# Kernel tuning notes

Hardware: AMD Instinct MI355X
Metric: run time of the kernel (lower is better)

The kernel has to match this reference:

```python
import jax, jax.numpy as jnp
import numpy as np

N, E = 50000, 800000
IN, H1, H2, HEADS, EMB = 128, 32, 32, 4, 128
NEG_SLOPE = 0.2  # DGL GATConv default leaky_relu slope


def setup_inputs() -> dict:
    key = jax.random.key(0)
    ks = jax.random.split(key, 14)
    s = 0.05
    return {
        "x": jax.random.normal(ks[0], (N, IN), jnp.float32),
        "src": jax.random.randint(ks[1], (E,), 0, N, jnp.int32),
        "dst": jax.random.randint(ks[2], (E,), 0, N, jnp.int32),
        "W1": jax.random.normal(ks[3], (IN, HEADS * H1), jnp.float32) * s,
        "al1": jax.random.normal(ks[4], (HEADS, H1), jnp.float32) * s,
        "ar1": jax.random.normal(ks[5], (HEADS, H1), jnp.float32) * s,
        "b1": jnp.zeros((HEADS * H1,), jnp.float32),
        "W2": jax.random.normal(ks[6], (HEADS * H1, HEADS * H2), jnp.float32) * s,
        "al2": jax.random.normal(ks[7], (HEADS, H2), jnp.float32) * s,
        "ar2": jax.random.normal(ks[8], (HEADS, H2), jnp.float32) * s,
        "b2": jnp.zeros((HEADS * H2,), jnp.float32),
        "Wp": jax.random.normal(ks[9], (HEADS * H2, EMB), jnp.float32) * s,
        "bp": jnp.zeros((EMB,), jnp.float32),
    }


def gat_layer(x, W, al, ar, b, src, dst, heads, d_out):
    n = x.shape[0]
    feat = (x @ W).reshape(n, heads, d_out)            # [N,H,D]
    el = (feat * al).sum(-1)                           # [N,H]
    er = (feat * ar).sum(-1)                           # [N,H]
    e = jax.nn.leaky_relu(el[src] + er[dst], NEG_SLOPE)  # [E,H]
    # edge softmax over destination segments
    m = jax.ops.segment_max(e, dst, num_segments=n)    # [N,H] (-inf for empty)
    ex = jnp.exp(e - m[dst])                           # [E,H]
    z = jax.ops.segment_sum(ex, dst, num_segments=n)   # [N,H]
    alpha = ex / z[dst]                                # [E,H]
    msg = alpha[:, :, None] * feat[src]                # [E,H,D]
    out = jax.ops.segment_sum(msg, dst, num_segments=n)  # [N,H,D]
    return out + b.reshape(1, heads, d_out)


def reference(x, src, dst, W1, al1, ar1, b1, W2, al2, ar2, b2, Wp, bp):
    h = gat_layer(x, W1, al1, ar1, b1, src, dst, HEADS, H1).reshape(N, -1)
    h = gat_layer(h, W2, al2, ar2, b2, src, dst, HEADS, H2).reshape(N, -1)
    out = h @ Wp + bp
    return (h, out)
```

## Files before the change

### kernel.cpp

```cpp
#include <hip/hip_runtime.h>
#include <hip/hip_bf16.h>

#define N_NODES 50000
#define HEADS 4
#define DHEAD 32
#define F 128
#define NEG_SLOPE 0.2f

typedef unsigned int uint;
typedef unsigned short ushort;
typedef __attribute__((ext_vector_type(8))) short bf16x8;
typedef __attribute__((ext_vector_type(4))) float f32x4;

__device__ __forceinline__ float bf2f(ushort u) {
    union { uint i; float f; } c; c.i = ((uint)u) << 16; return c.f;
}
__device__ __forceinline__ ushort f2bf(float f) {
    union { float f; uint i; } c; c.f = f;
    uint u = c.i + 0x7FFF + ((c.i >> 16) & 1);
    return (ushort)(u >> 16);
}

__global__ void rank_hist_kernel(const int* __restrict__ dst, int* __restrict__ counts,
                                 int* __restrict__ rank, int E) {
    int i = blockIdx.x * 256 + threadIdx.x;
    if (i < E) rank[i] = atomicAdd(&counts[dst[i]], 1);
}

__global__ __launch_bounds__(256) void scanA_kernel(const int* __restrict__ counts,
                                                    int* __restrict__ local_sc,
                                                    int* __restrict__ partials, int N) {
    int i = blockIdx.x * 256 + threadIdx.x;
    int v = (i < N) ? counts[i] : 0;
    int lane = threadIdx.x & 63;
    int w = threadIdx.x >> 6;
    int x = v;
#pragma unroll
    for (int off = 1; off < 64; off <<= 1) {
        int t = __shfl_up(x, off);
        if (lane >= off) x += t;
    }
    __shared__ int wsum[4];
    if (lane == 63) wsum[w] = x;
    __syncthreads();
    int wpre = 0;
#pragma unroll
    for (int k = 0; k < 4; k++)
        if (k < w) wpre += wsum[k];
    if (i < N) local_sc[i] = x - v + wpre;
    if (threadIdx.x == 255) partials[blockIdx.x] = wpre + x;
}

__global__ void scanB_kernel(int* __restrict__ partials, int NP) {
    int tid = threadIdx.x;
    int v = (tid < NP) ? partials[tid] : 0;
    int lane = tid & 63;
    int w = tid >> 6;
    int x = v;
#pragma unroll
    for (int off = 1; off < 64; off <<= 1) {
        int t = __shfl_up(x, off);
        if (lane >= off) x += t;
    }
    __shared__ int wsum[4];
    if (lane == 63) wsum[w] = x;
    __syncthreads();
    int wpre = 0;
#pragma unroll
    for (int k = 0; k < 4; k++)
        if (k < w) wpre += wsum[k];
    if (tid < NP) partials[tid] = x - v + wpre;
}

__global__ __launch_bounds__(256) void scanC_kernel(int* __restrict__ offs,
                                                    const int* __restrict__ partials,
                                                    int N, int E) {
    int i = blockIdx.x * 256 + threadIdx.x;
    if (i < N) offs[i] += partials[blockIdx.x];
    if (i == 0) offs[N] = E;
}

__global__ void posfix_kernel(const int* __restrict__ dst, const int* __restrict__ offs,
                              int* __restrict__ rank, int E) {
    int i = blockIdx.x * 256 + threadIdx.x;
    if (i < E) rank[i] += offs[dst[i]];
}

#define SCH 2048
__global__ __launch_bounds__(256) void scatter_ranged_kernel(
    const int* __restrict__ src, const int* __restrict__ pos,
    int* __restrict__ csr_src, int E) {
    int range = blockIdx.x & 7;
    int chunk = blockIdx.x >> 3;
    int base = chunk * SCH + threadIdx.x;
    int lo = (int)(((long long)range * E) >> 3);
    int hi = (int)(((long long)(range + 1) * E) >> 3);
#pragma unroll
    for (int k = 0; k < SCH / 256; k++) {
        int i = base + k * 256;
        if (i < E) {
            int p = pos[i];
            if (p >= lo && p < hi) csr_src[p] = src[i];
        }
    }
}

__global__ __launch_bounds__(256) void wtrans_kernel(const float* __restrict__ W1,
                                                     const float* __restrict__ W2,
                                                     const float* __restrict__ Wp,
                                                     ushort* __restrict__ WT) {
    const float* W = (blockIdx.x == 0) ? W1 : (blockIdx.x == 1) ? W2 : Wp;
    ushort* T = WT + (size_t)blockIdx.x * 128 * 128;
    for (int i = threadIdx.x; i < 128 * 128; i += 256) {
        int r = i >> 7, c = i & 127;
        T[c * 128 + r] = f2bf(W[i]);
    }
}

template <bool A_FP32, bool OUT_BF16, bool BIAS>
__global__ __launch_bounds__(256) void mfma_gemm_kernel(
    const void* __restrict__ Av, const ushort* __restrict__ BT,
    const float* __restrict__ bias, void* __restrict__ Cv, int M) {
    int wid = threadIdx.x >> 6;
    int lane = threadIdx.x & 63;
    int row0 = blockIdx.x * 64 + wid * 16;
    int rsub = lane & 15;
    int kg = lane >> 4;
    int row = row0 + rsub;
    int rowc = (row < M) ? row : (M - 1);

    bf16x8 af[4];
    if (A_FP32) {
        const float* A = (const float*)Av;
        const float* ap = A + (size_t)rowc * 128 + kg * 8;
#pragma unroll
        for (int ks = 0; ks < 4; ks++) {
            float4 lo = *(const float4*)(ap + ks * 32);
            float4 hi = *(const float4*)(ap + ks * 32 + 4);
            bf16x8 v;
            v[0] = (short)f2bf(lo.x); v[1] = (short)f2bf(lo.y);
            v[2] = (short)f2bf(lo.z); v[3] = (short)f2bf(lo.w);
            v[4] = (short)f2bf(hi.x); v[5] = (short)f2bf(hi.y);
            v[6] = (short)f2bf(hi.z); v[7] = (short)f2bf(hi.w);
            af[ks] = v;
        }
    } else {
        const ushort* A = (const ushort*)Av;
        const ushort* ap = A + (size_t)rowc * 128 + kg * 8;
#pragma unroll
        for (int ks = 0; ks < 4; ks++) af[ks] = *(const bf16x8*)(ap + ks * 32);
    }

    f32x4 acc[8];
#pragma unroll
    for (int ct = 0; ct < 8; ct++) acc[ct] = (f32x4){0.f, 0.f, 0.f, 0.f};

    const ushort* bp = BT + (size_t)rsub * 128 + kg * 8;
#pragma unroll
    for (int ks = 0; ks < 4; ks++) {
#pragma unroll
        for (int ct = 0; ct < 8; ct++) {
            bf16x8 bf = *(const bf16x8*)(bp + (size_t)ct * 16 * 128 + ks * 32);
            acc[ct] = __builtin_amdgcn_mfma_f32_16x16x32_bf16(af[ks], bf, acc[ct], 0, 0, 0);
        }
    }

    if (row0 >= M) return;
#pragma unroll
    for (int ct = 0; ct < 8; ct++) {
        int col = ct * 16 + rsub;
        float bv = BIAS ? bias[col] : 0.f;
#pragma unroll
        for (int r = 0; r < 4; r++) {
            int gr = row0 + kg * 4 + r;
            if (gr < M) {
                float v = acc[ct][r] + bv;
                if (OUT_BF16) ((ushort*)Cv)[(size_t)gr * 128 + col] = f2bf(v);
                else          ((float*)Cv)[(size_t)gr * 128 + col] = v;
            }
        }
    }
}

__global__ void eler_kernel(const ushort* __restrict__ featb, const float* __restrict__ al,
                            const float* __restrict__ ar, float* __restrict__ el,
                            float* __restrict__ er, int NH) {
    int idx = blockIdx.x * 256 + threadIdx.x;
    if (idx >= NH) return;
    int h = idx & 3;
    const ushort* f = featb + (size_t)idx * 32;
    const float* a_l = al + h * 32;
    const float* a_r = ar + h * 32;
    float sl = 0.f, sr = 0.f;
#pragma unroll
    for (int q = 0; q < 4; q++) {
        uint4 fv = *(const uint4*)(f + q * 8);
        float fx[8] = {bf2f(fv.x & 0xFFFF), bf2f(fv.x >> 16),
                       bf2f(fv.y & 0xFFFF), bf2f(fv.y >> 16),
                       bf2f(fv.z & 0xFFFF), bf2f(fv.z >> 16),
                       bf2f(fv.w & 0xFFFF), bf2f(fv.w >> 16)};
        float4 lv0 = *(const float4*)(a_l + q * 8);
        float4 lv1 = *(const float4*)(a_l + q * 8 + 4);
        float4 rv0 = *(const float4*)(a_r + q * 8);
        float4 rv1 = *(const float4*)(a_r + q * 8 + 4);
        sl += fx[0] * lv0.x + fx[1] * lv0.y + fx[2] * lv0.z + fx[3] * lv0.w
            + fx[4] * lv1.x + fx[5] * lv1.y + fx[6] * lv1.z + fx[7] * lv1.w;
        sr += fx[0] * rv0.x + fx[1] * rv0.y + fx[2] * rv0.z + fx[3] * rv0.w
            + fx[4] * rv1.x + fx[5] * rv1.y + fx[6] * rv1.z + fx[7] * rv1.w;
    }
    el[idx] = sl;
    er[idx] = sr;
}

template <bool F32OUT>
__global__ __launch_bounds__(256) void aggregate_kernel(
    const ushort* __restrict__ featb, const float* __restrict__ el,
    const float* __restrict__ er, const float* __restrict__ bias,
    const int* __restrict__ offsets, const int* __restrict__ csr_src,
    void* __restrict__ outv, int N) {
    int tid = threadIdx.x;
    int gl = tid & 15;
    int lane = tid & 63;
    int n = blockIdx.x * 16 + (tid >> 4);
    if (n >= N) return;
    int start = offsets[n], end = offsets[n + 1];

    float4 erv = *(const float4*)(er + (size_t)n * 4);
    float er_h[4] = {erv.x, erv.y, erv.z, erv.w};

    float m[4], s[4];
#pragma unroll
    for (int h = 0; h < 4; h++) { m[h] = -1e30f; s[h] = 0.f; }

    for (int e = start + gl; e < end; e += 16) {
        int sv = csr_src[e];
        float4 ev = *(const float4*)(el + (size_t)sv * 4);
        float elh[4] = {ev.x, ev.y, ev.z, ev.w};
#pragma unroll
        for (int h = 0; h < 4; h++) {
            float v = elh[h] + er_h[h];
            v = (v >= 0.f) ? v : NEG_SLOPE * v;
            float mn = fmaxf(m[h], v);
            s[h] = s[h] * __expf(m[h] - mn) + __expf(v - mn);
            m[h] = mn;
        }
    }
#pragma unroll
    for (int off = 1; off < 16; off <<= 1) {
#pragma unroll
        for (int h = 0; h < 4; h++) {
            float mo = __shfl_xor(m[h], off);
            float so = __shfl_xor(s[h], off);
            float mn = fmaxf(m[h], mo);
            s[h] = s[h] * __expf(m[h] - mn) + so * __expf(mo - mn);
            m[h] = mn;
        }
    }

    int h0 = gl >> 2;
    int j  = gl & 3;
    int c0 = gl * 8;
    float mh  = (h0 & 2) ? ((h0 & 1) ? m[3] : m[2]) : ((h0 & 1) ? m[1] : m[0]);
    float sh  = (h0 & 2) ? ((h0 & 1) ? s[3] : s[2]) : ((h0 & 1) ? s[1] : s[0]);
    float erh = (h0 & 2) ? ((h0 & 1) ? er_h[3] : er_h[2]) : ((h0 & 1) ? er_h[1] : er_h[0]);
    float rzh = (end > start) ? 1.0f / sh : 0.f;
    int bidx = lane & 60;

    float acc[8] = {};
    for (int e = start; e < end; e += 4) {
        int rem = end - e;
        int ej = e + ((j < rem) ? j : 0);
        int svj = csr_src[ej];
        float v = el[(size_t)svj * 4 + h0] + erh;
        v = (v >= 0.f) ? v : NEG_SLOPE * v;
        float a = __expf(v - mh) * rzh;
        if (j >= rem) a = 0.f;
#pragma unroll
        for (int jj = 0; jj < 4; jj++) {
            float ajj = __shfl(a, bidx | jj);
            int svjj  = __shfl(svj, bidx | jj);
            uint4 f0 = *(const uint4*)(featb + (size_t)svjj * 128 + c0);
            acc[0] = fmaf(ajj, bf2f(f0.x & 0xFFFF), acc[0]);
            acc[1] = fmaf(ajj, bf2f(f0.x >> 16),    acc[1]);
            acc[2] = fmaf(ajj, bf2f(f0.y & 0xFFFF), acc[2]);
            acc[3] = fmaf(ajj, bf2f(f0.y >> 16),    acc[3]);
            acc[4] = fmaf(ajj, bf2f(f0.z & 0xFFFF), acc[4]);
            acc[5] = fmaf(ajj, bf2f(f0.z >> 16),    acc[5]);
            acc[6] = fmaf(ajj, bf2f(f0.w & 0xFFFF), acc[6]);
            acc[7] = fmaf(ajj, bf2f(f0.w >> 16),    acc[7]);
        }
    }

    float4 b0 = *(const float4*)(bias + c0);
    float4 b1 = *(const float4*)(bias + c0 + 4);
    float o[8];
    o[0] = acc[0] + b0.x; o[1] = acc[1] + b0.y; o[2] = acc[2] + b0.z; o[3] = acc[3] + b0.w;
    o[4] = acc[4] + b1.x; o[5] = acc[5] + b1.y; o[6] = acc[6] + b1.z; o[7] = acc[7] + b1.w;
    if (F32OUT) {
        float* outf = (float*)outv;
        float4 w0, w1;
        w0.x = o[0]; w0.y = o[1]; w0.z = o[2]; w0.w = o[3];
        w1.x = o[4]; w1.y = o[5]; w1.z = o[6]; w1.w = o[7];
        *(float4*)(outf + (size_t)n * 128 + c0) = w0;
        *(float4*)(outf + (size_t)n * 128 + c0 + 4) = w1;
    } else {
        ushort* outb = (ushort*)outv;
        uint4 p;
        p.x = (uint)f2bf(o[0]) | ((uint)f2bf(o[1]) << 16);
        p.y = (uint)f2bf(o[2]) | ((uint)f2bf(o[3]) << 16);
        p.z = (uint)f2bf(o[4]) | ((uint)f2bf(o[5]) << 16);
        p.w = (uint)f2bf(o[6]) | ((uint)f2bf(o[7]) << 16);
        *(uint4*)(outb + (size_t)n * 128 + c0) = p;
    }
}

extern "C" void kernel_launch(void* const* d_in, const int* in_sizes, int n_in,
                              void* d_out, int out_size, void* d_ws, size_t ws_size,
                              hipStream_t stream) {
    const float* x   = (const float*)d_in[0];
    const int*   src = (const int*)d_in[1];
    const int*   dst = (const int*)d_in[2];
    const float* W1  = (const float*)d_in[3];
    const float* al1 = (const float*)d_in[4];
    const float* ar1 = (const float*)d_in[5];
    const float* b1  = (const float*)d_in[6];
    const float* W2  = (const float*)d_in[7];
    const float* al2 = (const float*)d_in[8];
    const float* ar2 = (const float*)d_in[9];
    const float* b2  = (const float*)d_in[10];
    const float* Wp  = (const float*)d_in[11];
    const float* bp  = (const float*)d_in[12];

    const int N = in_sizes[0] / F;
    const int E = in_sizes[1];

    float* h_out = (float*)d_out;
    float* p_out = h_out + (size_t)N * F;

    char* w = (char*)d_ws;
    ushort* featb   = (ushort*)w;
    ushort* h1b     = featb + (size_t)N * F;
    float* el       = (float*)(h1b + (size_t)N * F);
    float* er       = el + (size_t)N * 4;
    int*   offs     = (int*)(er + (size_t)N * 4);
    int*   counts   = offs + (N + 1);
    int*   rank     = counts + N;
    int*   csrsrc   = rank + E;
    int*   partials = csrsrc + E;
    ushort* WT      = (ushort*)(partials + 256);

    const int NB = (N + 255) / 256;
    const int EB = (E + 255) / 256;

    hipMemsetAsync(counts, 0, (size_t)N * 4, stream);
    rank_hist_kernel<<<EB, 256, 0, stream>>>(dst, counts, rank, E);
    scanA_kernel<<<NB, 256, 0, stream>>>(counts, offs, partials, N);
    scanB_kernel<<<1, 256, 0, stream>>>(partials, NB);
    scanC_kernel<<<NB, 256, 0, stream>>>(offs, partials, N, E);
    posfix_kernel<<<EB, 256, 0, stream>>>(dst, offs, rank, E);
    scatter_ranged_kernel<<<8 * ((E + SCH - 1) / SCH), 256, 0, stream>>>(src, rank, csrsrc, E);

    wtrans_kernel<<<3, 256, 0, stream>>>(W1, W2, Wp, WT);
    ushort* WT1 = WT;
    ushort* WT2 = WT + 128 * 128;
    ushort* WTp = WT + 2 * 128 * 128;

    int ggrid = (N + 63) / 64;
    int agrid = (N + 15) / 16;

    mfma_gemm_kernel<true, true, false><<<ggrid, 256, 0, stream>>>(x, WT1, nullptr, featb, N);
    eler_kernel<<<(N * 4 + 255) / 256, 256, 0, stream>>>(featb, al1, ar1, el, er, N * 4);
    aggregate_kernel<false><<<agrid, 256, 0, stream>>>(featb, el, er, b1, offs, csrsrc, h1b, N);

    mfma_gemm_kernel<false, true, false><<<ggrid, 256, 0, stream>>>(h1b, WT2, nullptr, featb, N);
    eler_kernel<<<(N * 4 + 255) / 256, 256, 0, stream>>>(featb, al2, ar2, el, er, N * 4);
    aggregate_kernel<true><<<agrid, 256, 0, stream>>>(featb, el, er, b2, offs, csrsrc, h_out, N);

    mfma_gemm_kernel<true, false, true><<<ggrid, 256, 0, stream>>>(h_out, WTp, bp, p_out, N);
}
```

Baseline: 254.1 us.

## Cache per-edge logits in registers for low-degree nodes in GAT aggregation

For nodes with degree at most 32, the aggregate kernel now keeps each edge's source index and leaky-relu logit in registers from the softmax pass. The aggregation pass then reads them with shuffles instead of reloading csr_src and el for every edge, and processes two edges per iteration so two feature loads are in flight at once. High-degree nodes use a simplified per-edge loop. The cost is more registers, extra shuffles per edge, and divergent code paths.

```diff
diff --git a/kernel.cpp b/kernel.cpp
--- a/kernel.cpp
+++ b/kernel.cpp
@@ -19,6 +19,9 @@
     union { float f; uint i; } c; c.f = f;
     uint u = c.i + 0x7FFF + ((c.i >> 16) & 1);
     return (ushort)(u >> 16);
+}
+__device__ __forceinline__ float sel4(int h, float a, float b, float c, float d) {
+    return (h & 2) ? ((h & 1) ? d : c) : ((h & 1) ? b : a);
 }
 
 __global__ void rank_hist_kernel(const int* __restrict__ dst, int* __restrict__ counts,
@@ -221,9 +224,11 @@
     int tid = threadIdx.x;
     int gl = tid & 15;
     int lane = tid & 63;
+    int gbase = lane & 48;
     int n = blockIdx.x * 16 + (tid >> 4);
     if (n >= N) return;
     int start = offsets[n], end = offsets[n + 1];
+    int deg = end - start;
 
     float4 erv = *(const float4*)(er + (size_t)n * 4);
     float er_h[4] = {erv.x, erv.y, erv.z, erv.w};
@@ -232,19 +237,55 @@
 #pragma unroll
     for (int h = 0; h < 4; h++) { m[h] = -1e30f; s[h] = 0.f; }
 
-    for (int e = start + gl; e < end; e += 16) {
-        int sv = csr_src[e];
-        float4 ev = *(const float4*)(el + (size_t)sv * 4);
-        float elh[4] = {ev.x, ev.y, ev.z, ev.w};
-#pragma unroll
-        for (int h = 0; h < 4; h++) {
-            float v = elh[h] + er_h[h];
-            v = (v >= 0.f) ? v : NEG_SLOPE * v;
-            float mn = fmaxf(m[h], v);
-            s[h] = s[h] * __expf(m[h] - mn) + __expf(v - mn);
-            m[h] = mn;
-        }
-    }
+    int sv0 = 0, sv1 = 0;
+    float a0[4] = {0.f, 0.f, 0.f, 0.f};
+    float a1[4] = {0.f, 0.f, 0.f, 0.f};
+
+    bool fast = (deg <= 32);
+    if (fast) {
+        if (gl < deg) {
+            sv0 = csr_src[start + gl];
+            float4 ev = *(const float4*)(el + (size_t)sv0 * 4);
+            float vv[4] = {ev.x, ev.y, ev.z, ev.w};
+#pragma unroll
+            for (int h = 0; h < 4; h++) {
+                float v = vv[h] + er_h[h];
+                v = (v >= 0.f) ? v : NEG_SLOPE * v;
+                a0[h] = v;
+                m[h] = v;
+                s[h] = 1.f;
+            }
+        }
+        if (16 + gl < deg) {
+            sv1 = csr_src[start + 16 + gl];
+            float4 ev = *(const float4*)(el + (size_t)sv1 * 4);
+            float vv[4] = {ev.x, ev.y, ev.z, ev.w};
+#pragma unroll
+            for (int h = 0; h < 4; h++) {
+                float v = vv[h] + er_h[h];
+                v = (v >= 0.f) ? v : NEG_SLOPE * v;
+                a1[h] = v;
+                float mn = fmaxf(m[h], v);
+                s[h] = s[h] * __expf(m[h] - mn) + __expf(v - mn);
+                m[h] = mn;
+            }
+        }
+    } else {
+        for (int e = start + gl; e < end; e += 16) {
+            int sv = csr_src[e];
+            float4 ev = *(const float4*)(el + (size_t)sv * 4);
+            float vv[4] = {ev.x, ev.y, ev.z, ev.w};
+#pragma unroll
+            for (int h = 0; h < 4; h++) {
+                float v = vv[h] + er_h[h];
+                v = (v >= 0.f) ? v : NEG_SLOPE * v;
+                float mn = fmaxf(m[h], v);
+                s[h] = s[h] * __expf(m[h] - mn) + __expf(v - mn);
+                m[h] = mn;
+            }
+        }
+    }
+
 #pragma unroll
     for (int off = 1; off < 16; off <<= 1) {
 #pragma unroll
@@ -257,37 +298,96 @@
         }
     }
 
+    float rz[4];
+#pragma unroll
+    for (int h = 0; h < 4; h++) rz[h] = (deg > 0) ? 1.0f / s[h] : 0.f;
+
     int h0 = gl >> 2;
-    int j  = gl & 3;
     int c0 = gl * 8;
-    float mh  = (h0 & 2) ? ((h0 & 1) ? m[3] : m[2]) : ((h0 & 1) ? m[1] : m[0]);
-    float sh  = (h0 & 2) ? ((h0 & 1) ? s[3] : s[2]) : ((h0 & 1) ? s[1] : s[0]);
-    float erh = (h0 & 2) ? ((h0 & 1) ? er_h[3] : er_h[2]) : ((h0 & 1) ? er_h[1] : er_h[0]);
-    float rzh = (end > start) ? 1.0f / sh : 0.f;
-    int bidx = lane & 60;
-
     float acc[8] = {};
-    for (int e = start; e < end; e += 4) {
-        int rem = end - e;
-        int ej = e + ((j < rem) ? j : 0);
-        int svj = csr_src[ej];
-        float v = el[(size_t)svj * 4 + h0] + erh;
-        v = (v >= 0.f) ? v : NEG_SLOPE * v;
-        float a = __expf(v - mh) * rzh;
-        if (j >= rem) a = 0.f;
-#pragma unroll
-        for (int jj = 0; jj < 4; jj++) {
-            float ajj = __shfl(a, bidx | jj);
-            int svjj  = __shfl(svj, bidx | jj);
-            uint4 f0 = *(const uint4*)(featb + (size_t)svjj * 128 + c0);
-            acc[0] = fmaf(ajj, bf2f(f0.x & 0xFFFF), acc[0]);
-            acc[1] = fmaf(ajj, bf2f(f0.x >> 16),    acc[1]);
-            acc[2] = fmaf(ajj, bf2f(f0.y & 0xFFFF), acc[2]);
-            acc[3] = fmaf(ajj, bf2f(f0.y >> 16),    acc[3]);
-            acc[4] = fmaf(ajj, bf2f(f0.z & 0xFFFF), acc[4]);
-            acc[5] = fmaf(ajj, bf2f(f0.z >> 16),    acc[5]);
-            acc[6] = fmaf(ajj, bf2f(f0.w & 0xFFFF), acc[6]);
-            acc[7] = fmaf(ajj, bf2f(f0.w >> 16),    acc[7]);
+
+    if (fast) {
+#pragma unroll
+        for (int h = 0; h < 4; h++) {
+            a0[h] = (gl < deg)      ? __expf(a0[h] - m[h]) * rz[h] : 0.f;
+            a1[h] = (16 + gl < deg) ? __expf(a1[h] - m[h]) * rz[h] : 0.f;
+        }
+        int jj = 0;
+        for (; jj + 1 < deg; jj += 2) {
+            bool sec0 = jj >= 16;
+            int sl0 = gbase | (jj & 15);
+            int sva   = __shfl(sec0 ? sv1 : sv0, sl0);
+            float t0  = __shfl(sec0 ? a1[0] : a0[0], sl0);
+            float t1  = __shfl(sec0 ? a1[1] : a0[1], sl0);
+            float t2  = __shfl(sec0 ? a1[2] : a0[2], sl0);
+            float t3  = __shfl(sec0 ? a1[3] : a0[3], sl0);
+            float aa = sel4(h0, t0, t1, t2, t3);
+
+            bool sec1 = (jj + 1) >= 16;
+            int sl1 = gbase | ((jj + 1) & 15);
+            int svb   = __shfl(sec1 ? sv1 : sv0, sl1);
+            float u0  = __shfl(sec1 ? a1[0] : a0[0], sl1);
+            float u1  = __shfl(sec1 ? a1[1] : a0[1], sl1);
+            float u2  = __shfl(sec1 ? a1[2] : a0[2], sl1);
+            float u3  = __shfl(sec1 ? a1[3] : a0[3], sl1);
+            float ab = sel4(h0, u0, u1, u2, u3);
+
+            uint4 fa = *(const uint4*)(featb + (size_t)sva * 128 + c0);
+            uint4 fb = *(const uint4*)(featb + (size_t)svb * 128 + c0);
+            acc[0] = fmaf(aa, bf2f(fa.x & 0xFFFF), acc[0]);
+            acc[1] = fmaf(aa, bf2f(fa.x >> 16),    acc[1]);
+            acc[2] = fmaf(aa, bf2f(fa.y & 0xFFFF), acc[2]);
+            acc[3] = fmaf(aa, bf2f(fa.y >> 16),    acc[3]);
+            acc[4] = fmaf(aa, bf2f(fa.z & 0xFFFF), acc[4]);
+            acc[5] = fmaf(aa, bf2f(fa.z >> 16),    acc[5]);
+            acc[6] = fmaf(aa, bf2f(fa.w & 0xFFFF), acc[6]);
+            acc[7] = fmaf(aa, bf2f(fa.w >> 16),    acc[7]);
+            acc[0] = fmaf(ab, bf2f(fb.x & 0xFFFF), acc[0]);
+            acc[1] = fmaf(ab, bf2f(fb.x >> 16),    acc[1]);
+            acc[2] = fmaf(ab, bf2f(fb.y & 0xFFFF), acc[2]);
+            acc[3] = fmaf(ab, bf2f(fb.y >> 16),    acc[3]);
+            acc[4] = fmaf(ab, bf2f(fb.z & 0xFFFF), acc[4]);
+            acc[5] = fmaf(ab, bf2f(fb.z >> 16),    acc[5]);
+            acc[6] = fmaf(ab, bf2f(fb.w & 0xFFFF), acc[6]);
+            acc[7] = fmaf(ab, bf2f(fb.w >> 16),    acc[7]);
+        }
+        if (jj < deg) {
+            bool sec0 = jj >= 16;
+            int sl0 = gbase | (jj & 15);
+            int sva   = __shfl(sec0 ? sv1 : sv0, sl0);
+            float t0  = __shfl(sec0 ? a1[0] : a0[0], sl0);
+            float t1  = __shfl(sec0 ? a1[1] : a0[1], sl0);
+            float t2  = __shfl(sec0 ? a1[2] : a0[2], sl0);
+            float t3  = __shfl(sec0 ? a1[3] : a0[3], sl0);
+            float aa = sel4(h0, t0, t1, t2, t3);
+            uint4 fa = *(const uint4*)(featb + (size_t)sva * 128 + c0);
+            acc[0] = fmaf(aa, bf2f(fa.x & 0xFFFF), acc[0]);
+            acc[1] = fmaf(aa, bf2f(fa.x >> 16),    acc[1]);
+            acc[2] = fmaf(aa, bf2f(fa.y & 0xFFFF), acc[2]);
+            acc[3] = fmaf(aa, bf2f(fa.y >> 16),    acc[3]);
+            acc[4] = fmaf(aa, bf2f(fa.z & 0xFFFF), acc[4]);
+            acc[5] = fmaf(aa, bf2f(fa.z >> 16),    acc[5]);
+            acc[6] = fmaf(aa, bf2f(fa.w & 0xFFFF), acc[6]);
+            acc[7] = fmaf(aa, bf2f(fa.w >> 16),    acc[7]);
+        }
+    } else {
+        float mh  = sel4(h0, m[0], m[1], m[2], m[3]);
+        float erh = sel4(h0, er_h[0], er_h[1], er_h[2], er_h[3]);
+        float rzh = sel4(h0, rz[0], rz[1], rz[2], rz[3]);
+        for (int e = start; e < end; e++) {
+            int sv = csr_src[e];
+            float v = el[(size_t)sv * 4 + h0] + erh;
+            v = (v >= 0.f) ? v : NEG_SLOPE * v;
+            float a = __expf(v - mh) * rzh;
+            uint4 f0 = *(const uint4*)(featb + (size_t)sv * 128 + c0);
+            acc[0] = fmaf(a, bf2f(f0.x & 0xFFFF), acc[0]);
+            acc[1] = fmaf(a, bf2f(f0.x >> 16),    acc[1]);
+            acc[2] = fmaf(a, bf2f(f0.y & 0xFFFF), acc[2]);
+            acc[3] = fmaf(a, bf2f(f0.y >> 16),    acc[3]);
+            acc[4] = fmaf(a, bf2f(f0.z & 0xFFFF), acc[4]);
+            acc[5] = fmaf(a, bf2f(f0.z >> 16),    acc[5]);
+            acc[6] = fmaf(a, bf2f(f0.w & 0xFFFF), acc[6]);
+            acc[7] = fmaf(a, bf2f(f0.w >> 16),    acc[7]);
         }
     }
 
```

Result: slower. 270.3 us (+6.4%).
